# Performance work log

Measured on AMD Instinct MI355X. Metric: run time of the kernel, lower is better.

## Reference

```python
import jax, jax.numpy as jnp
import numpy as np

NUM_LAYERS = 4
B, L, D = 8, 512, 512
H, F = 8, 2048
HD = D // H
EPS = 1e-5


def _layernorm(x, g, b):
    mu = jnp.mean(x, axis=-1, keepdims=True)
    var = jnp.var(x, axis=-1, keepdims=True)
    return (x - mu) * jax.lax.rsqrt(var + EPS) * g + b


def setup_inputs() -> dict:
    key = jax.random.key(0)
    ks = jax.random.split(key, 14)
    s = 0.02
    return {
        "src": jax.random.normal(ks[0], (B, L, D), dtype=jnp.float32),
        "Wqkv": jax.random.normal(ks[1], (NUM_LAYERS, 3 * D, D), dtype=jnp.float32) * s,
        "bqkv": jnp.zeros((NUM_LAYERS, 3 * D), dtype=jnp.float32),
        "Wo": jax.random.normal(ks[2], (NUM_LAYERS, D, D), dtype=jnp.float32) * s,
        "bo": jnp.zeros((NUM_LAYERS, D), dtype=jnp.float32),
        "W1": jax.random.normal(ks[3], (NUM_LAYERS, F, D), dtype=jnp.float32) * s,
        "b1": jnp.zeros((NUM_LAYERS, F), dtype=jnp.float32),
        "W2": jax.random.normal(ks[4], (NUM_LAYERS, D, F), dtype=jnp.float32) * s,
        "b2": jnp.zeros((NUM_LAYERS, D), dtype=jnp.float32),
        "g1": jnp.ones((NUM_LAYERS, D), dtype=jnp.float32),
        "be1": jnp.zeros((NUM_LAYERS, D), dtype=jnp.float32),
        "g2": jnp.ones((NUM_LAYERS, D), dtype=jnp.float32),
        "be2": jnp.zeros((NUM_LAYERS, D), dtype=jnp.float32),
    }


def reference(src, Wqkv, bqkv, Wo, bo, W1, b1, W2, b2, g1, be1, g2, be2):
    x = src
    attns = []
    scale = 1.0 / np.sqrt(HD).astype(np.float32)
    for i in range(NUM_LAYERS):
        # --- self attention (need_weights=True, average_attn_weights=False) ---
        qkv = x @ Wqkv[i].T + bqkv[i]                      # [B,L,3D]
        q, k, v = jnp.split(qkv, 3, axis=-1)
        q = q.reshape(B, L, H, HD).transpose(0, 2, 1, 3)   # [B,H,L,hd]
        k = k.reshape(B, L, H, HD).transpose(0, 2, 1, 3)
        v = v.reshape(B, L, H, HD).transpose(0, 2, 1, 3)
        scores = jnp.einsum("bhld,bhsd->bhls", q * scale, k)
        attn = jax.nn.softmax(scores, axis=-1)             # [B,H,L,S]
        attns.append(attn)
        ctx = jnp.einsum("bhls,bhsd->bhld", attn, v)
        ctx = ctx.transpose(0, 2, 1, 3).reshape(B, L, D)
        attn_out = ctx @ Wo[i].T + bo[i]
        # --- post-norm residual + FFN ---
        x = _layernorm(x + attn_out, g1[i], be1[i])
        ff = jax.nn.relu(x @ W1[i].T + b1[i]) @ W2[i].T + b2[i]
        x = _layernorm(x + ff, g2[i], be2[i])
    return x, jnp.stack(attns)  # ([B,L,D], [num_layers,B,H,L,S])
```

## Files before the change

### kernel.cpp

```cpp
#include <hip/hip_runtime.h>
#include <hip/hip_bf16.h>

#define B_ 8
#define L_ 512
#define D_ 512
#define H_ 8
#define F_ 2048
#define NL_ 4
#define BL 4096
#define EPS_ 1e-5f

typedef __bf16 bf16_t;
typedef bf16_t bf16x8 __attribute__((ext_vector_type(8)));
typedef float f32x4 __attribute__((ext_vector_type(4)));
typedef unsigned short u16x4 __attribute__((ext_vector_type(4)));

__device__ __forceinline__ unsigned short f2b_rn(float f) {
  unsigned u = __builtin_bit_cast(unsigned, f);
  u = (u + 0x7fffu + ((u >> 16) & 1u)) >> 16;
  return (unsigned short)u;
}

__device__ __forceinline__ void gload_lds16(const unsigned short* g, unsigned short* l) {
  __builtin_amdgcn_global_load_lds(
      (const __attribute__((address_space(1))) void*)g,
      (__attribute__((address_space(3))) void*)l, 16, 0, 0);
}

template<int BM, int BN, int MT, int NT>
__global__ __launch_bounds__(256)
void gemm_bt(const unsigned short* __restrict__ A, int lda, long sAo, long sAi,
             const unsigned short* __restrict__ Bm, int ldb, long sBo, long sBi,
             float* __restrict__ Cf, unsigned short* __restrict__ Cb, int ldc,
             long sCo, long sCi,
             const float* __restrict__ bias, int K, float scale, int relu, int zi)
{
  static_assert(BM == MT * 32 && BN == NT * 32, "waves are 2x2");
  __shared__ unsigned short As[2][BM * 32];
  __shared__ unsigned short Bs[2][BN * 32];
  const int tid  = threadIdx.x;
  const int lane = tid & 63;
  const int wave = tid >> 6;
  const int wm = (wave >> 1) * (MT * 16);
  const int wn = (wave & 1) * (NT * 16);
  int bx = blockIdx.x, by = blockIdx.y;
  if (gridDim.z == 1 && (gridDim.x & 7) == 0) {
    const int gx = gridDim.x, cx = gx >> 3;
    const int lid = by * gx + bx;
    const int xcd = lid & 7;
    const int t = lid >> 3;
    bx = xcd * cx + (t % cx);
    by = t / cx;
  }
  const int m0 = bx * BM;
  const int n0 = by * BN;
  const int z  = blockIdx.z;
  const long offA = (long)(z / zi) * sAo + (long)(z % zi) * sAi;
  const long offB = (long)(z / zi) * sBo + (long)(z % zi) * sBi;
  const long offC = (long)(z / zi) * sCo + (long)(z % zi) * sCi;

  const unsigned short* Ab = A + offA + (long)m0 * lda;
  const unsigned short* Bb = Bm + offB + (long)n0 * ldb;

  auto stage = [&](int buf, int k0) {
#pragma unroll
    for (int j = 0; j < BM / 64; ++j) {
      int c = tid + j * 256;
      int r = c >> 2, cc = (c & 3) * 8;
      gload_lds16(Ab + (long)r * lda + (k0 + cc), &As[buf][c * 8]);
    }
#pragma unroll
    for (int j = 0; j < BN / 64; ++j) {
      int c = tid + j * 256;
      int r = c >> 2, cc = (c & 3) * 8;
      gload_lds16(Bb + (long)r * ldb + (k0 + cc), &Bs[buf][c * 8]);
    }
  };

  f32x4 acc[MT][NT] = {};

  stage(0, 0);
  __syncthreads();
  int cur = 0;
  for (int k0 = 0; k0 < K; k0 += 32) {
    if (k0 + 32 < K) stage(cur ^ 1, k0 + 32);
    bf16x8 af[MT], bfr[NT];
#pragma unroll
    for (int mt = 0; mt < MT; ++mt)
      af[mt] = *(const bf16x8*)(&As[cur][(wm + mt * 16 + (lane & 15)) * 32 + (lane >> 4) * 8]);
#pragma unroll
    for (int nt = 0; nt < NT; ++nt)
      bfr[nt] = *(const bf16x8*)(&Bs[cur][(wn + nt * 16 + (lane & 15)) * 32 + (lane >> 4) * 8]);
#pragma unroll
    for (int mt = 0; mt < MT; ++mt)
#pragma unroll
      for (int nt = 0; nt < NT; ++nt)
        acc[mt][nt] = __builtin_amdgcn_mfma_f32_16x16x32_bf16(af[mt], bfr[nt], acc[mt][nt], 0, 0, 0);
    __syncthreads();
    cur ^= 1;
  }

#pragma unroll
  for (int nt = 0; nt < NT; ++nt) {
    const int col = n0 + wn + nt * 16 + (lane & 15);
    const float bb = bias ? bias[col] : 0.f;
#pragma unroll
    for (int mt = 0; mt < MT; ++mt) {
#pragma unroll
      for (int r = 0; r < 4; ++r) {
        const int row = m0 + wm + mt * 16 + (lane >> 4) * 4 + r;
        float v = acc[mt][nt][r] * scale + bb;
        if (relu) v = fmaxf(v, 0.f);
        const long o = offC + (long)row * ldc + col;
        if (Cf) Cf[o] = v;
        if (Cb) Cb[o] = f2b_rn(v);
      }
    }
  }
}

__global__ __launch_bounds__(256)
void attn_fused(const unsigned short* __restrict__ qkv,
                float* __restrict__ attnf,
                unsigned short* __restrict__ ctxb) {
  __shared__ __align__(16) unsigned short Qs[64 * 64];
  __shared__ __align__(16) unsigned short KP[512 * 64];
  __shared__ __align__(16) unsigned short VT[64 * 512];
  const int tid = threadIdx.x, lane = tid & 63, wave = tid >> 6;
  const int lo4 = lane & 15, hi4 = lane >> 4;
  int bxr = blockIdx.x, byr = blockIdx.y;
  {
    const int lid = byr * 8 + bxr;
    const int xcd = lid & 7;
    const int t = lid >> 3;
    byr = xcd * 8 + (t & 7);
    bxr = t >> 3;
  }
  const int q0 = bxr * 64;
  const int z = byr, b = z >> 3, h = z & 7;
  const unsigned short* qbase = qkv + (long)b * 512 * 1536 + h * 64;
  const unsigned short* kbase = qbase + 512;
  const unsigned short* vbase = qbase + 1024;

  bf16x8 vreg[16];
#pragma unroll
  for (int j = 0; j < 16; ++j) {
    const int d8 = j >> 1;
    const int s = (j & 1) * 256 + tid;
    vreg[j] = *(const bf16x8*)(vbase + (long)s * 1536 + d8 * 8);
  }

#pragma unroll
  for (int j = 0; j < 2; ++j) {
    int c = tid + j * 256;
    int r = c >> 3, cc = (c & 7) * 8;
    gload_lds16(qbase + (long)(q0 + r) * 1536 + cc, &Qs[c * 8]);
  }
#pragma unroll
  for (int j = 0; j < 16; ++j) {
    int c = tid + j * 256;
    int r = c >> 3, ch = (c & 7) ^ (r & 7);
    gload_lds16(kbase + (long)r * 1536 + ch * 8, &KP[c * 8]);
  }
  __syncthreads();

  const bf16x8 qf0 = *(const bf16x8*)&Qs[(wave * 16 + lo4) * 64 + hi4 * 8];
  const bf16x8 qf1 = *(const bf16x8*)&Qs[(wave * 16 + lo4) * 64 + 32 + hi4 * 8];

  f32x4 acc[32];
#pragma unroll
  for (int st = 0; st < 32; ++st) {
    const int n = st * 16 + lo4;
    const int sw = lo4 & 7;
    f32x4 a = {};
    const bf16x8 k0f = *(const bf16x8*)&KP[n * 64 + ((hi4 ^ sw) * 8)];
    const bf16x8 k1f = *(const bf16x8*)&KP[n * 64 + (((hi4 + 4) ^ sw) * 8)];
    a = __builtin_amdgcn_mfma_f32_16x16x32_bf16(k0f, qf0, a, 0, 0, 0);
    a = __builtin_amdgcn_mfma_f32_16x16x32_bf16(k1f, qf1, a, 0, 0, 0);
    acc[st] = a;
  }

  float mx = -1e30f;
#pragma unroll
  for (int st = 0; st < 32; ++st)
#pragma unroll
    for (int r = 0; r < 4; ++r) {
      acc[st][r] *= 0.125f;
      mx = fmaxf(mx, acc[st][r]);
    }
  mx = fmaxf(mx, __shfl_xor(mx, 16));
  mx = fmaxf(mx, __shfl_xor(mx, 32));
  float sm = 0.f;
#pragma unroll
  for (int st = 0; st < 32; ++st)
#pragma unroll
    for (int r = 0; r < 4; ++r) {
      const float e = __expf(acc[st][r] - mx);
      acc[st][r] = e;
      sm += e;
    }
  sm += __shfl_xor(sm, 16);
  sm += __shfl_xor(sm, 32);
  const float inv = 1.f / sm;

  __syncthreads();

#pragma unroll
  for (int j = 0; j < 16; ++j) {
    const int d8 = j >> 1;
    const int s = (j & 1) * 256 + tid;
#pragma unroll
    for (int jj = 0; jj < 8; ++jj) {
      const int d = d8 * 8 + jj;
      VT[(d * 512 + s) ^ ((d & 7) << 3)] = ((const unsigned short*)&vreg[j])[jj];
    }
  }

  const int q = wave * 16 + lo4;
#pragma unroll
  for (int st = 0; st < 32; ++st) {
    u16x4 pb;
#pragma unroll
    for (int r = 0; r < 4; ++r) {
      acc[st][r] *= inv;
      pb[r] = f2b_rn(acc[st][r]);
    }
    *(u16x4*)&KP[(q * 512 + st * 16 + hi4 * 4) ^ ((q & 7) << 3)] = pb;
  }
  __syncthreads();

  float* aout = attnf + (long)z * 262144 + (long)(q0 + q) * 512;
#pragma unroll
  for (int st = 0; st < 32; ++st)
    __builtin_nontemporal_store(acc[st], (f32x4*)(aout + st * 16 + hi4 * 4));

  const int wq = (wave >> 1) * 32, wd = (wave & 1) * 32;
  f32x4 acc2[2][2] = {};
#pragma unroll
  for (int k0 = 0; k0 < 512; k0 += 32) {
    bf16x8 vf[2], pf[2];
#pragma unroll
    for (int mt = 0; mt < 2; ++mt) {
      const int d = wd + mt * 16 + lo4;
      vf[mt] = *(const bf16x8*)&VT[(d * 512 + k0 + hi4 * 8) ^ ((d & 7) << 3)];
    }
#pragma unroll
    for (int nt = 0; nt < 2; ++nt) {
      const int m = wq + nt * 16 + lo4;
      pf[nt] = *(const bf16x8*)&KP[(m * 512 + k0 + hi4 * 8) ^ ((m & 7) << 3)];
    }
#pragma unroll
    for (int mt = 0; mt < 2; ++mt)
#pragma unroll
      for (int nt = 0; nt < 2; ++nt)
        acc2[mt][nt] = __builtin_amdgcn_mfma_f32_16x16x32_bf16(vf[mt], pf[nt], acc2[mt][nt], 0, 0, 0);
  }

#pragma unroll
  for (int nt = 0; nt < 2; ++nt) {
    const int qq = q0 + wq + nt * 16 + lo4;
    unsigned short* cb = ctxb + ((long)(b * 512 + qq)) * 512 + h * 64;
#pragma unroll
    for (int mt = 0; mt < 2; ++mt) {
      u16x4 o;
#pragma unroll
      for (int r = 0; r < 4; ++r) o[r] = f2b_rn(acc2[mt][nt][r]);
      *(u16x4*)&cb[wd + mt * 16 + hi4 * 4] = o;
    }
  }
}

__global__ __launch_bounds__(128)
void resid_ln(const float* __restrict__ a, const float* __restrict__ b,
              const float* __restrict__ g, const float* __restrict__ be,
              float* __restrict__ outf, unsigned short* __restrict__ outb) {
  const long row = blockIdx.x;
  const int t = threadIdx.x;
  const int wave = t >> 6, lane = t & 63;
  const f32x4 va = *(const f32x4*)&a[row * 512 + t * 4];
  const f32x4 vb = *(const f32x4*)&b[row * 512 + t * 4];
  f32x4 v;
  float s = 0.f, s2 = 0.f;
#pragma unroll
  for (int i = 0; i < 4; ++i) { v[i] = va[i] + vb[i]; s += v[i]; s2 += v[i] * v[i]; }
  for (int o = 32; o > 0; o >>= 1) { s += __shfl_down(s, o); s2 += __shfl_down(s2, o); }
  __shared__ float red[4];
  if (lane == 0) { red[wave] = s; red[2 + wave] = s2; }
  __syncthreads();
  s = red[0] + red[1];
  s2 = red[2] + red[3];
  const float mu  = s * (1.f / 512.f);
  const float var = s2 * (1.f / 512.f) - mu * mu;
  const float ri = rsqrtf(var + EPS_);
  const f32x4 vg = *(const f32x4*)&g[t * 4];
  const f32x4 ve = *(const f32x4*)&be[t * 4];
  f32x4 y;
  u16x4 yb;
#pragma unroll
  for (int i = 0; i < 4; ++i) { y[i] = (v[i] - mu) * ri * vg[i] + ve[i]; yb[i] = f2b_rn(y[i]); }
  *(f32x4*)&outf[row * 512 + t * 4] = y;
  *(u16x4*)&outb[row * 512 + t * 4] = yb;
}

__global__ void f2b_arr(const float* __restrict__ in, unsigned short* __restrict__ out, long n4) {
  long i = (long)blockIdx.x * 256 + threadIdx.x;
  const long stride = (long)gridDim.x * 256;
  for (; i < n4; i += stride) {
    const f32x4 v = *(const f32x4*)&in[i * 4];
    u16x4 o;
#pragma unroll
    for (int k = 0; k < 4; ++k) o[k] = f2b_rn(v[k]);
    *(u16x4*)&out[i * 4] = o;
  }
}

__global__ void copy_conv(const float* __restrict__ in, float* __restrict__ outf,
                          unsigned short* __restrict__ outb, long n4) {
  long i = (long)blockIdx.x * 256 + threadIdx.x;
  const long stride = (long)gridDim.x * 256;
  for (; i < n4; i += stride) {
    const f32x4 v = *(const f32x4*)&in[i * 4];
    u16x4 o;
#pragma unroll
    for (int k = 0; k < 4; ++k) o[k] = f2b_rn(v[k]);
    *(f32x4*)&outf[i * 4] = v;
    *(u16x4*)&outb[i * 4] = o;
  }
}

extern "C" void kernel_launch(void* const* d_in, const int* in_sizes, int n_in,
                              void* d_out, int out_size, void* d_ws, size_t ws_size,
                              hipStream_t stream) {
  const float* src  = (const float*)d_in[0];
  const float* Wqkv = (const float*)d_in[1];
  const float* bqkv = (const float*)d_in[2];
  const float* Wo   = (const float*)d_in[3];
  const float* bo   = (const float*)d_in[4];
  const float* W1   = (const float*)d_in[5];
  const float* b1   = (const float*)d_in[6];
  const float* W2   = (const float*)d_in[7];
  const float* b2   = (const float*)d_in[8];
  const float* g1   = (const float*)d_in[9];
  const float* be1  = (const float*)d_in[10];
  const float* g2   = (const float*)d_in[11];
  const float* be2  = (const float*)d_in[12];

  char* p = (char*)d_ws;
  auto take = [&](size_t bytes) { void* r = (void*)p; p += (bytes + 255) & ~(size_t)255; return r; };
  float* x        = (float*)take((size_t)BL * 512 * 4);
  float* x1       = (float*)take((size_t)BL * 512 * 4);
  float* attn_out = (float*)take((size_t)BL * 512 * 4);
  float* ff2      = (float*)take((size_t)BL * 512 * 4);
  unsigned short* xbf    = (unsigned short*)take((size_t)BL * 512 * 2);
  unsigned short* qkvbf  = (unsigned short*)take((size_t)BL * 1536 * 2);
  unsigned short* ctxbf  = (unsigned short*)take((size_t)BL * 512 * 2);
  unsigned short* ff1bf  = (unsigned short*)take((size_t)BL * 2048 * 2);
  unsigned short* Wqkvb  = (unsigned short*)take((size_t)4 * 1536 * 512 * 2);
  unsigned short* Wob    = (unsigned short*)take((size_t)4 * 512 * 512 * 2);
  unsigned short* W1b    = (unsigned short*)take((size_t)4 * 2048 * 512 * 2);
  unsigned short* W2b    = (unsigned short*)take((size_t)4 * 512 * 2048 * 2);

  f2b_arr<<<1024, 256, 0, stream>>>(Wqkv, Wqkvb, 4L * 1536 * 512 / 4);
  f2b_arr<<<512,  256, 0, stream>>>(Wo,   Wob,   4L * 512 * 512 / 4);
  f2b_arr<<<1024, 256, 0, stream>>>(W1,   W1b,   4L * 2048 * 512 / 4);
  f2b_arr<<<1024, 256, 0, stream>>>(W2,   W2b,   4L * 512 * 2048 / 4);
  copy_conv<<<1024, 256, 0, stream>>>(src, x, xbf, (long)BL * 512 / 4);

  float* out_x    = (float*)d_out;
  float* out_attn = out_x + (size_t)BL * 512;

  for (int i = 0; i < NL_; ++i) {
    gemm_bt<64, 128, 2, 4><<<dim3(BL / 64, 1536 / 128, 1), 256, 0, stream>>>(
        xbf, 512, 0, 0, Wqkvb + (size_t)i * 1536 * 512, 512, 0, 0,
        nullptr, qkvbf, 1536, 0, 0, bqkv + (size_t)i * 1536, 512, 1.f, 0, 1);

    float* attnL = out_attn + (size_t)i * 64 * 512 * 512;
    attn_fused<<<dim3(8, 64), 256, 0, stream>>>(qkvbf, attnL, ctxbf);

    gemm_bt<128, 64, 4, 2><<<dim3(32, 8, 1), 256, 0, stream>>>(
        ctxbf, 512, 0, 0, Wob + (size_t)i * 512 * 512, 512, 0, 0,
        attn_out, nullptr, 512, 0, 0, bo + (size_t)i * 512, 512, 1.f, 0, 1);

    resid_ln<<<BL, 128, 0, stream>>>(x, attn_out, g1 + (size_t)i * 512, be1 + (size_t)i * 512, x1, xbf);

    gemm_bt<128, 128, 4, 4><<<dim3(32, 16, 1), 256, 0, stream>>>(
        xbf, 512, 0, 0, W1b + (size_t)i * 2048 * 512, 512, 0, 0,
        nullptr, ff1bf, 2048, 0, 0, b1 + (size_t)i * 2048, 512, 1.f, 1, 1);

    gemm_bt<128, 64, 4, 2><<<dim3(32, 8, 1), 256, 0, stream>>>(
        ff1bf, 2048, 0, 0, W2b + (size_t)i * 512 * 2048, 2048, 0, 0,
        ff2, nullptr, 512, 0, 0, b2 + (size_t)i * 512, 2048, 1.f, 0, 1);

    resid_ln<<<BL, 128, 0, stream>>>(x1, ff2, g2 + (size_t)i * 512, be2 + (size_t)i * 512,
                                     (i == 3) ? out_x : x, xbf);
  }
}
```

Before: 797.9 us.

## Fuse output-projection and FFN2 GEMMs with residual add and LayerNorm

Adds a gemm_ln kernel in which each block computes a 16-row by 512-column output tile, so a whole row is available for the residual add, bias and LayerNorm. It replaces the Wo and W2 GEMMs plus the two separate resid_ln launches, removing the fp32 intermediate round trips through global memory and two launches per layer. In exchange each block streams the full 512-column weight panel from global memory for only 16 rows, giving low weight reuse, only 256 blocks, and large shared memory use (about 98KB) that limits occupancy.

```diff
diff --git a/kernel.cpp b/kernel.cpp
--- a/kernel.cpp
+++ b/kernel.cpp
@@ -120,6 +120,104 @@
 }
 
 __global__ __launch_bounds__(256)
+void gemm_ln(const unsigned short* __restrict__ A, int lda,
+             const unsigned short* __restrict__ Bw,
+             const float* __restrict__ res,
+             const float* __restrict__ bias,
+             const float* __restrict__ g, const float* __restrict__ be,
+             float* __restrict__ outf, unsigned short* __restrict__ outb,
+             int K)
+{
+  __shared__ __align__(16) unsigned short As[2][16 * 32];
+  __shared__ __align__(16) unsigned short Bs[2][512 * 32];
+  __shared__ __align__(16) float Y[16 * 512];
+  const int tid = threadIdx.x, lane = tid & 63, wave = tid >> 6;
+  const int lo4 = lane & 15, hi4 = lane >> 4;
+  const int bx = (blockIdx.x & 7) * 32 + (blockIdx.x >> 3);
+  const int m0 = bx * 16;
+  const unsigned short* Ab = A + (long)m0 * lda;
+
+  auto stage = [&](int buf, int k0) {
+    if (wave == 0)
+      gload_lds16(Ab + (long)(lane >> 2) * lda + (k0 + (lane & 3) * 8), &As[buf][lane * 8]);
+#pragma unroll
+    for (int j = 0; j < 8; ++j) {
+      int c = tid + j * 256;
+      int r = c >> 2, cc = (c & 3) * 8;
+      gload_lds16(Bw + (long)r * K + (k0 + cc), &Bs[buf][c * 8]);
+    }
+  };
+
+  f32x4 acc[8] = {};
+  stage(0, 0);
+  __syncthreads();
+  int cur = 0;
+  for (int k0 = 0; k0 < K; k0 += 32) {
+    if (k0 + 32 < K) stage(cur ^ 1, k0 + 32);
+    const bf16x8 af = *(const bf16x8*)&As[cur][lo4 * 32 + hi4 * 8];
+#pragma unroll
+    for (int nt = 0; nt < 8; ++nt) {
+      const bf16x8 bfr = *(const bf16x8*)&Bs[cur][(wave * 128 + nt * 16 + lo4) * 32 + hi4 * 8];
+      acc[nt] = __builtin_amdgcn_mfma_f32_16x16x32_bf16(af, bfr, acc[nt], 0, 0, 0);
+    }
+    __syncthreads();
+    cur ^= 1;
+  }
+
+#pragma unroll
+  for (int nt = 0; nt < 8; ++nt) {
+    const int col = wave * 128 + nt * 16 + lo4;
+#pragma unroll
+    for (int r = 0; r < 4; ++r)
+      Y[(hi4 * 4 + r) * 512 + col] = acc[nt][r];
+  }
+  __syncthreads();
+
+  const int row = tid >> 4, c16 = tid & 15;
+  const long grow = (long)(m0 + row) * 512;
+  f32x4 v[8];
+  float s = 0.f, s2 = 0.f;
+#pragma unroll
+  for (int j = 0; j < 8; ++j) {
+    const int col = c16 * 4 + j * 64;
+    const f32x4 yv = *(const f32x4*)&Y[row * 512 + col];
+    const f32x4 bb = *(const f32x4*)&bias[col];
+    const f32x4 rr = *(const f32x4*)&res[grow + col];
+    f32x4 t4;
+#pragma unroll
+    for (int i = 0; i < 4; ++i) {
+      t4[i] = yv[i] + bb[i] + rr[i];
+      s += t4[i];
+      s2 += t4[i] * t4[i];
+    }
+    v[j] = t4;
+  }
+#pragma unroll
+  for (int msk = 1; msk < 16; msk <<= 1) {
+    s  += __shfl_xor(s, msk);
+    s2 += __shfl_xor(s2, msk);
+  }
+  const float mu  = s * (1.f / 512.f);
+  const float var = s2 * (1.f / 512.f) - mu * mu;
+  const float ri  = rsqrtf(var + EPS_);
+#pragma unroll
+  for (int j = 0; j < 8; ++j) {
+    const int col = c16 * 4 + j * 64;
+    const f32x4 vg = *(const f32x4*)&g[col];
+    const f32x4 ve = *(const f32x4*)&be[col];
+    f32x4 y;
+    u16x4 yb;
+#pragma unroll
+    for (int i = 0; i < 4; ++i) {
+      y[i] = (v[j][i] - mu) * ri * vg[i] + ve[i];
+      yb[i] = f2b_rn(y[i]);
+    }
+    *(f32x4*)&outf[grow + col] = y;
+    *(u16x4*)&outb[grow + col] = yb;
+  }
+}
+
+__global__ __launch_bounds__(256)
 void attn_fused(const unsigned short* __restrict__ qkv,
                 float* __restrict__ attnf,
                 unsigned short* __restrict__ ctxb) {
@@ -268,38 +366,6 @@
       *(u16x4*)&cb[wd + mt * 16 + hi4 * 4] = o;
     }
   }
-}
-
-__global__ __launch_bounds__(128)
-void resid_ln(const float* __restrict__ a, const float* __restrict__ b,
-              const float* __restrict__ g, const float* __restrict__ be,
-              float* __restrict__ outf, unsigned short* __restrict__ outb) {
-  const long row = blockIdx.x;
-  const int t = threadIdx.x;
-  const int wave = t >> 6, lane = t & 63;
-  const f32x4 va = *(const f32x4*)&a[row * 512 + t * 4];
-  const f32x4 vb = *(const f32x4*)&b[row * 512 + t * 4];
-  f32x4 v;
-  float s = 0.f, s2 = 0.f;
-#pragma unroll
-  for (int i = 0; i < 4; ++i) { v[i] = va[i] + vb[i]; s += v[i]; s2 += v[i] * v[i]; }
-  for (int o = 32; o > 0; o >>= 1) { s += __shfl_down(s, o); s2 += __shfl_down(s2, o); }
-  __shared__ float red[4];
-  if (lane == 0) { red[wave] = s; red[2 + wave] = s2; }
-  __syncthreads();
-  s = red[0] + red[1];
-  s2 = red[2] + red[3];
-  const float mu  = s * (1.f / 512.f);
-  const float var = s2 * (1.f / 512.f) - mu * mu;
-  const float ri = rsqrtf(var + EPS_);
-  const f32x4 vg = *(const f32x4*)&g[t * 4];
-  const f32x4 ve = *(const f32x4*)&be[t * 4];
-  f32x4 y;
-  u16x4 yb;
-#pragma unroll
-  for (int i = 0; i < 4; ++i) { y[i] = (v[i] - mu) * ri * vg[i] + ve[i]; yb[i] = f2b_rn(y[i]); }
-  *(f32x4*)&outf[row * 512 + t * 4] = y;
-  *(u16x4*)&outb[row * 512 + t * 4] = yb;
 }
 
 __global__ void f2b_arr(const float* __restrict__ in, unsigned short* __restrict__ out, long n4) {
@@ -349,8 +415,6 @@
   auto take = [&](size_t bytes) { void* r = (void*)p; p += (bytes + 255) & ~(size_t)255; return r; };
   float* x        = (float*)take((size_t)BL * 512 * 4);
   float* x1       = (float*)take((size_t)BL * 512 * 4);
-  float* attn_out = (float*)take((size_t)BL * 512 * 4);
-  float* ff2      = (float*)take((size_t)BL * 512 * 4);
   unsigned short* xbf    = (unsigned short*)take((size_t)BL * 512 * 2);
   unsigned short* qkvbf  = (unsigned short*)take((size_t)BL * 1536 * 2);
   unsigned short* ctxbf  = (unsigned short*)take((size_t)BL * 512 * 2);
@@ -377,21 +441,16 @@
     float* attnL = out_attn + (size_t)i * 64 * 512 * 512;
     attn_fused<<<dim3(8, 64), 256, 0, stream>>>(qkvbf, attnL, ctxbf);
 
-    gemm_bt<128, 64, 4, 2><<<dim3(32, 8, 1), 256, 0, stream>>>(
-        ctxbf, 512, 0, 0, Wob + (size_t)i * 512 * 512, 512, 0, 0,
-        attn_out, nullptr, 512, 0, 0, bo + (size_t)i * 512, 512, 1.f, 0, 1);
-
-    resid_ln<<<BL, 128, 0, stream>>>(x, attn_out, g1 + (size_t)i * 512, be1 + (size_t)i * 512, x1, xbf);
+    gemm_ln<<<256, 256, 0, stream>>>(
+        ctxbf, 512, Wob + (size_t)i * 512 * 512, x, bo + (size_t)i * 512,
+        g1 + (size_t)i * 512, be1 + (size_t)i * 512, x1, xbf, 512);
 
     gemm_bt<128, 128, 4, 4><<<dim3(32, 16, 1), 256, 0, stream>>>(
         xbf, 512, 0, 0, W1b + (size_t)i * 2048 * 512, 512, 0, 0,
         nullptr, ff1bf, 2048, 0, 0, b1 + (size_t)i * 2048, 512, 1.f, 1, 1);
 
-    gemm_bt<128, 64, 4, 2><<<dim3(32, 8, 1), 256, 0, stream>>>(
-        ff1bf, 2048, 0, 0, W2b + (size_t)i * 512 * 2048, 2048, 0, 0,
-        ff2, nullptr, 512, 0, 0, b2 + (size_t)i * 512, 2048, 1.f, 0, 1);
-
-    resid_ln<<<BL, 128, 0, stream>>>(x1, ff2, g2 + (size_t)i * 512, be2 + (size_t)i * 512,
-                                     (i == 3) ? out_x : x, xbf);
-  }
-}
+    gemm_ln<<<256, 256, 0, stream>>>(
+        ff1bf, 2048, W2b + (size_t)i * 512 * 2048, x1, b2 + (size_t)i * 512,
+        g2 + (size_t)i * 512, be2 + (size_t)i * 512, (i == 3) ? out_x : x, xbf, 2048);
+  }
+}
```

New measurement: 938.2 us. +17.6%, slower.
